# Optimization experiments

Hardware: AMD Instinct MI355X
Metric: run time of the kernel (lower is better)

## Reference

```python
import jax, jax.numpy as jnp
from jax import lax
import numpy as np

EPS = 1e-5  # BatchNorm eps


def setup_inputs() -> dict:
    key = jax.random.key(0)
    ks = jax.random.split(key, 4)
    T, B, C = 256, 128, 1024
    L, H, NCLS = 6, 1024, 1000
    x = jax.random.normal(ks[0], (T, B, C), dtype=jnp.float32)
    W = jax.random.normal(ks[1], (L, C, H), dtype=jnp.float32) * (1.0 / np.sqrt(C))
    b = jnp.zeros((L, H), dtype=jnp.float32)
    gamma = jnp.ones((L, H), dtype=jnp.float32)
    beta = jnp.zeros((L, H), dtype=jnp.float32)
    u = jax.random.uniform(ks[2], (L, H), dtype=jnp.float32)  # recurrent weights in (0, U_bound~1)
    Wc = jax.random.normal(ks[3], (H, NCLS), dtype=jnp.float32) * (1.0 / np.sqrt(H))
    bc = jnp.zeros((NCLS,), dtype=jnp.float32)
    return {"x": x, "W": W, "b": b, "gamma": gamma, "beta": beta, "u": u, "Wc": Wc, "bc": bc}


def _layer(h, Wl, bl, gl, betal, ul):
    # per-timestep dense projection: [T,B,Cin] @ [Cin,H]
    z = jnp.einsum('tbi,ih->tbh', h, Wl) + bl
    # BN over (time, batch) per channel (bn_before, training-mode batch stats)
    mean = jnp.mean(z, axis=(0, 1))
    var = jnp.var(z, axis=(0, 1))
    z = (z - mean) * (gl / jnp.sqrt(var + EPS)) + betal
    # IndRNN diagonal recurrence: h_t = relu(z_t + u * h_{t-1}), h_0 = 0
    T, B, H = z.shape
    def step(hprev, zt):
        hnew = jax.nn.relu(zt + ul * hprev)
        return hnew, hnew
    _, hs = lax.scan(step, jnp.zeros((B, H), dtype=z.dtype), z)
    return hs


def reference(x, W, b, gamma, beta, u, Wc, bc):
    h = x
    for l in range(W.shape[0]):
        h = _layer(h, W[l], b[l], gamma[l], beta[l], u[l])
    # classifier on last timestep
    return h[-1] @ Wc + bc
```

## Files before the change

### kernel.cpp

```cpp
#include <hip/hip_runtime.h>
#include <hip/hip_bf16.h>

#define T_DIM 256
#define B_DIM 128
#define C_DIM 1024
#define H_DIM 1024
#define L_DIM 6
#define NC_DIM 1000
#define M_DIM (T_DIM * B_DIM)
#define BH_DIM (B_DIM * H_DIM)

typedef __attribute__((ext_vector_type(8))) short bf16x8;
typedef __attribute__((ext_vector_type(4))) float f32x4;

__device__ __forceinline__ float bf2f(unsigned short u) {
  union { unsigned int i; float f; } v; v.i = ((unsigned int)u) << 16; return v.f;
}
__device__ __forceinline__ unsigned short f2bf(float f) {
  union { float f; unsigned int i; } v; v.f = f;
  unsigned int r = v.i + 0x7fffu + ((v.i >> 16) & 1u);
  return (unsigned short)(r >> 16);
}
__device__ __forceinline__ unsigned int pack2bf(float lo, float hi) {
  __hip_bfloat162 b2 = __float22bfloat162_rn(float2{lo, hi});
  union { __hip_bfloat162 b; unsigned int u; } cv; cv.b = b2; return cv.u;
}

__device__ __forceinline__ void gload_lds16(const void* g, void* l) {
  __builtin_amdgcn_global_load_lds(
      (const __attribute__((address_space(1))) unsigned int*)g,
      (__attribute__((address_space(3))) unsigned int*)l, 16, 0, 0);
}

__global__ __launch_bounds__(256) void f32_to_bf16_kernel(
    const float* __restrict__ in, unsigned short* __restrict__ out, int n4) {
  int stride = gridDim.x * blockDim.x;
  for (int i = blockIdx.x * blockDim.x + threadIdx.x; i < n4; i += stride) {
    float4 v = ((const float4*)in)[i];
    uint2 o; o.x = pack2bf(v.x, v.y); o.y = pack2bf(v.z, v.w);
    ((uint2*)out)[i] = o;
  }
}

__global__ __launch_bounds__(256) void wtrans_kernel(
    const float* __restrict__ W, unsigned short* __restrict__ Wt) {
  __shared__ float tile[32][33];
  int l = blockIdx.z;
  const float* Wl = W + (size_t)l * C_DIM * H_DIM;
  unsigned short* Wtl = Wt + (size_t)l * C_DIM * H_DIM;
  int h0 = blockIdx.x * 32, c0 = blockIdx.y * 32;
  int tx = threadIdx.x, ty = threadIdx.y;
#pragma unroll
  for (int i = 0; i < 32; i += 8)
    tile[ty + i][tx] = Wl[(size_t)(c0 + ty + i) * H_DIM + h0 + tx];
  __syncthreads();
#pragma unroll
  for (int i = 0; i < 32; i += 8)
    Wtl[(size_t)(h0 + ty + i) * C_DIM + c0 + tx] = f2bf(tile[tx][ty + i]);
}

#define NT 32

__global__ __launch_bounds__(512, 2) void gemm_kernel(
    const unsigned short* __restrict__ A, const unsigned short* __restrict__ Bt,
    unsigned short* __restrict__ Z, float* __restrict__ psum, float* __restrict__ psqs) {
  extern __shared__ char lds[];
  int bid = blockIdx.x;
  int swz = (bid & 7) * 32 + (bid >> 3);
  int tm0 = (swz >> 2) * 2;
  int tn = swz & 3;
  int tid = threadIdx.x;
  int wv = tid >> 6, ln = tid & 63;
  int wm = wv >> 2, wn = wv & 3;

  const char* Ap0 = (const char*)A + (size_t)tm0 * 256 * 2048;
  const char* Ap1 = Ap0 + (size_t)256 * 2048;
  const char* Bpanel = (const char*)Bt + (size_t)tn * 256 * 2048;

  int p0 = wv * 1024 + ln * 16;
  int l0 = p0 ^ (((p0 >> 7) & 3) << 4);
  size_t ro0 = (size_t)(p0 >> 6) * 2048 + (l0 & 63);
  size_t ro1 = (size_t)(128 + (p0 >> 6)) * 2048 + (l0 & 63);
  int sdst = wv * 1024;

  auto stage = [&](const char* Ap, int t) {
    char* base = lds + ((t & 3) * 32768);
    int kb = t * 64;
    gload_lds16(Ap + ro0 + kb, base + sdst);
    gload_lds16(Ap + ro1 + kb, base + 8192 + sdst);
    gload_lds16(Bpanel + ro0 + kb, base + 16384 + sdst);
    gload_lds16(Bpanel + ro1 + kb, base + 16384 + 8192 + sdst);
  };

  int frow = ln & 15;
  int fchunk = ((ln >> 4) ^ (frow >> 1)) & 3;
  int floff = frow * 64 + (fchunk << 4);

  f32x4 acc[8][4];

  bf16x8 bX[4], aP[4], aQ[4];
  auto readB_to = [&](int t, bf16x8* d) {
    const char* Bb = lds + ((t & 3) * 32768) + 16384 + wn * 4096;
#pragma unroll
    for (int n = 0; n < 4; ++n) d[n] = *(const bf16x8*)(Bb + n * 1024 + floff);
  };
  auto readA_to = [&](int t, int mq, bf16x8* d) {
    const char* Ab = lds + ((t & 3) * 32768) + wm * 8192 + mq * 4096;
#pragma unroll
    for (int i = 0; i < 4; ++i) d[i] = *(const bf16x8*)(Ab + i * 1024 + floff);
  };

  auto kloop = [&](const char* Ap) {
    f32x4 zero = {0.f, 0.f, 0.f, 0.f};
#pragma unroll
    for (int m = 0; m < 8; ++m)
#pragma unroll
      for (int n = 0; n < 4; ++n) acc[m][n] = zero;
    readB_to(0, bX); readA_to(0, 0, aP);
    for (int t = 0; t < NT; ++t) {
      readA_to(t, 1, aQ);
      if (t <= NT - 4) stage(Ap, t + 3);
      __builtin_amdgcn_s_setprio(1);
#pragma unroll
      for (int i = 0; i < 4; ++i)
#pragma unroll
        for (int n = 0; n < 4; ++n)
          acc[i][n] = __builtin_amdgcn_mfma_f32_16x16x32_bf16(aP[i], bX[n], acc[i][n], 0, 0, 0);
      __builtin_amdgcn_s_setprio(0);
      __builtin_amdgcn_s_setprio(1);
#pragma unroll
      for (int i = 0; i < 4; ++i)
#pragma unroll
        for (int n = 0; n < 4; ++n)
          acc[4 + i][n] = __builtin_amdgcn_mfma_f32_16x16x32_bf16(aQ[i], bX[n], acc[4 + i][n], 0, 0, 0);
      __builtin_amdgcn_s_setprio(0);
      if (t < NT - 1) {
        readB_to(t + 1, bX); readA_to(t + 1, 0, aP);
        if (t <= NT - 4) { asm volatile("s_waitcnt vmcnt(4)" ::: "memory"); }
        else             { asm volatile("s_waitcnt vmcnt(0)" ::: "memory"); }
        __builtin_amdgcn_s_barrier();
      }
    }
  };

  float* red = (float*)(lds + 3 * 32768);
  auto epilogue = [&](int tm) {
    float s[4], q[4];
#pragma unroll
    for (int n = 0; n < 4; ++n) {
      float sv = 0.f, qv = 0.f;
#pragma unroll
      for (int m = 0; m < 8; ++m)
#pragma unroll
        for (int r = 0; r < 4; ++r) {
          float v = acc[m][n][r];
          sv += v; qv += v * v;
        }
      s[n] = sv; q[n] = qv;
    }
#pragma unroll
    for (int n = 0; n < 4; ++n) {
      s[n] += __shfl_xor(s[n], 16); s[n] += __shfl_xor(s[n], 32);
      q[n] += __shfl_xor(q[n], 16); q[n] += __shfl_xor(q[n], 32);
    }
    if (ln < 16) {
#pragma unroll
      for (int n = 0; n < 4; ++n) {
        red[wm * 256 + wn * 64 + n * 16 + ln] = s[n];
        red[512 + wm * 256 + wn * 64 + n * 16 + ln] = q[n];
      }
    }
    __syncthreads();
    if (tid < 256) {
      psum[(size_t)tm * H_DIM + tn * 256 + tid] = red[tid] + red[256 + tid];
    } else {
      int c = tid - 256;
      psqs[(size_t)tm * H_DIM + tn * 256 + c] = red[512 + c] + red[768 + c];
    }
    __syncthreads();
    int r0 = tm * 256 + wm * 128 + ((ln >> 4) << 2);
    int c0 = tn * 256 + wn * 64 + (ln & 15);
#pragma unroll
    for (int m = 0; m < 8; ++m)
#pragma unroll
      for (int n = 0; n < 4; ++n) {
        unsigned short* zp = Z + (size_t)(r0 + m * 16) * H_DIM + c0 + n * 16;
#pragma unroll
        for (int r = 0; r < 4; ++r) zp[(size_t)r * H_DIM] = f2bf(acc[m][n][r]);
      }
  };

  stage(Ap0, 0); stage(Ap0, 1); stage(Ap0, 2);
  asm volatile("s_waitcnt vmcnt(4)" ::: "memory");
  __builtin_amdgcn_s_barrier();
  kloop(Ap0);
  __builtin_amdgcn_s_barrier();
  stage(Ap1, 0); stage(Ap1, 1); stage(Ap1, 2);
  epilogue(tm0);
  asm volatile("s_waitcnt vmcnt(4)" ::: "memory");
  __builtin_amdgcn_s_barrier();
  kloop(Ap1);
  __builtin_amdgcn_s_barrier();
  epilogue(tm0 + 1);
}

__global__ __launch_bounds__(256) void bn_finalize_kernel(
    const float* __restrict__ psum, const float* __restrict__ psqs,
    const float* __restrict__ gamma, const float* __restrict__ beta,
    float* __restrict__ ss) {
  __shared__ float sred[2][8][32];
  int c0 = blockIdx.x * 32;
  int cl = threadIdx.x & 31, jg = threadIdx.x >> 5;
  float s = 0.f, q = 0.f;
#pragma unroll
  for (int j = 0; j < 16; ++j) {
    size_t row = (size_t)(jg * 16 + j) * H_DIM + c0 + cl;
    s += psum[row];
    q += psqs[row];
  }
  sred[0][jg][cl] = s;
  sred[1][jg][cl] = q;
  __syncthreads();
  if (threadIdx.x < 32) {
    int c = threadIdx.x;
    float ts = 0.f, tq = 0.f;
#pragma unroll
    for (int g = 0; g < 8; ++g) { ts += sred[0][g][c]; tq += sred[1][g][c]; }
    const float invN = 1.0f / (float)M_DIM;
    float mean = ts * invN;
    float var = tq * invN - mean * mean;
    float sc = gamma[c0 + c] * rsqrtf(var + 1e-5f);
    ss[c0 + c] = sc;
    ss[H_DIM + c0 + c] = beta[c0 + c] - mean * sc;
  }
}

__global__ __launch_bounds__(256) void bn_recur_kernel(
    const unsigned short* __restrict__ Z, const float* __restrict__ ss,
    const float* __restrict__ u, unsigned short* __restrict__ Hout, int full) {
  int i2 = blockIdx.x * 256 + threadIdx.x;
  int h0 = (i2 & (H_DIM / 2 - 1)) * 2;
  float sc0 = ss[h0], sc1 = ss[h0 + 1];
  float sh0 = ss[H_DIM + h0], sh1 = ss[H_DIM + h0 + 1];
  float u0 = u[h0], u1 = u[h0 + 1];
  float hv0 = 0.f, hv1 = 0.f;

  const size_t ST = BH_DIM / 2;
  const unsigned int* Zt = (const unsigned int*)Z + i2;
  unsigned int* Ht = (unsigned int*)Hout + i2;

  unsigned int za[32], zb[32], ho[32];
#pragma unroll
  for (int j = 0; j < 32; ++j) za[j] = Zt[(size_t)j * ST];

#pragma unroll
  for (int blk = 0; blk < 4; ++blk) {
    int tA = blk * 64;
#pragma unroll
    for (int j = 0; j < 32; ++j) zb[j] = Zt[(size_t)(tA + 32 + j) * ST];
#pragma unroll
    for (int j = 0; j < 32; ++j) {
      unsigned int zz = za[j];
      float z0 = fmaf(bf2f((unsigned short)(zz & 0xffffu)), sc0, sh0);
      float z1 = fmaf(bf2f((unsigned short)(zz >> 16)), sc1, sh1);
      hv0 = fmaxf(fmaf(u0, hv0, z0), 0.f);
      hv1 = fmaxf(fmaf(u1, hv1, z1), 0.f);
      ho[j] = pack2bf(hv0, hv1);
    }
#pragma unroll
    for (int j = 0; j < 32; ++j)
      if (full || (tA + j) == T_DIM - 1) Ht[(size_t)(tA + j) * ST] = ho[j];
    if (blk < 3) {
#pragma unroll
      for (int j = 0; j < 32; ++j) za[j] = Zt[(size_t)(tA + 64 + j) * ST];
    }
#pragma unroll
    for (int j = 0; j < 32; ++j) {
      unsigned int zz = zb[j];
      float z0 = fmaf(bf2f((unsigned short)(zz & 0xffffu)), sc0, sh0);
      float z1 = fmaf(bf2f((unsigned short)(zz >> 16)), sc1, sh1);
      hv0 = fmaxf(fmaf(u0, hv0, z0), 0.f);
      hv1 = fmaxf(fmaf(u1, hv1, z1), 0.f);
      ho[j] = pack2bf(hv0, hv1);
    }
#pragma unroll
    for (int j = 0; j < 32; ++j)
      if (full || (tA + 32 + j) == T_DIM - 1) Ht[(size_t)(tA + 32 + j) * ST] = ho[j];
  }
}

__global__ __launch_bounds__(256) void classifier_kernel(
    const unsigned short* __restrict__ hlast, const float* __restrict__ Wc,
    const float* __restrict__ bc, float* __restrict__ out) {
  __shared__ float hs[H_DIM];
  int b = blockIdx.y;
  int n = blockIdx.x * 256 + threadIdx.x;
  for (int k = threadIdx.x; k < H_DIM; k += 256)
    hs[k] = bf2f(hlast[(size_t)b * H_DIM + k]);
  __syncthreads();
  if (n < NC_DIM) {
    float acc = bc[n];
#pragma unroll 8
    for (int k = 0; k < H_DIM; ++k)
      acc = fmaf(hs[k], Wc[(size_t)k * NC_DIM + n], acc);
    out[(size_t)b * NC_DIM + n] = acc;
  }
}

extern "C" void kernel_launch(void* const* d_in, const int* in_sizes, int n_in,
                              void* d_out, int out_size, void* d_ws, size_t ws_size,
                              hipStream_t stream) {
  const float* x     = (const float*)d_in[0];
  const float* W     = (const float*)d_in[1];
  const float* gamma = (const float*)d_in[3];
  const float* beta  = (const float*)d_in[4];
  const float* u     = (const float*)d_in[5];
  const float* Wc    = (const float*)d_in[6];
  const float* bc    = (const float*)d_in[7];
  float* out = (float*)d_out;

  const size_t CH = (size_t)C_DIM * H_DIM;
  const size_t MH = (size_t)M_DIM * H_DIM;
  char* p = (char*)d_ws;
  unsigned short* Wt = (unsigned short*)p; p += L_DIM * CH * sizeof(unsigned short);
  unsigned short* Ha = (unsigned short*)p; p += MH * sizeof(unsigned short);
  unsigned short* Hb = (unsigned short*)p; p += MH * sizeof(unsigned short);
  unsigned short* Z  = (unsigned short*)p; p += MH * sizeof(unsigned short);
  float* psum = (float*)p; p += 128 * H_DIM * sizeof(float);
  float* psqs = (float*)p; p += 128 * H_DIM * sizeof(float);
  float* ss   = (float*)p; p += 2 * H_DIM * sizeof(float);

  f32_to_bf16_kernel<<<2048, 256, 0, stream>>>(x, Ha, (int)(MH / 4));
  wtrans_kernel<<<dim3(H_DIM / 32, C_DIM / 32, L_DIM), dim3(32, 8), 0, stream>>>(W, Wt);

  unsigned short* cur = Ha;
  unsigned short* nxt = Hb;
  for (int l = 0; l < L_DIM; ++l) {
    gemm_kernel<<<256, 512, 131072, stream>>>(cur, Wt + (size_t)l * CH, Z, psum, psqs);
    bn_finalize_kernel<<<32, 256, 0, stream>>>(psum, psqs, gamma + (size_t)l * H_DIM,
                                               beta + (size_t)l * H_DIM, ss);
    bn_recur_kernel<<<BH_DIM / 512, 256, 0, stream>>>(Z, ss, u + (size_t)l * H_DIM, nxt,
                                                      (l < L_DIM - 1) ? 1 : 0);
    unsigned short* tmp = cur; cur = nxt; nxt = tmp;
  }
  classifier_kernel<<<dim3(4, B_DIM), 256, 0, stream>>>(
      cur + (size_t)(T_DIM - 1) * BH_DIM, Wc, bc, out);
}
```

Measured before the change: 694.3 us.

## Restructure GEMM into one tile per block with K=64 double-buffered quadrant pipeline

The GEMM kernel now computes one 256x256 output tile per block (512 blocks instead of 256 blocks each doing two M tiles). The K step grows to 64 with two LDS buffers of 64KB, replacing the earlier four 32KB buffers. Each K step is split into four MFMA quadrants interleaved with LDS fragment reads and half-panel global-to-LDS staging, separated by barriers and sched_barriers. A new XOR swizzle covers the 128-byte rows. The aim is better overlap of memory traffic with MFMA and fewer per-step waits, at the cost of many more barriers per iteration and less reuse of the B panel inside each block.

```diff
diff --git a/kernel.cpp b/kernel.cpp
--- a/kernel.cpp
+++ b/kernel.cpp
@@ -59,149 +59,156 @@
     Wtl[(size_t)(h0 + ty + i) * C_DIM + c0 + tx] = f2bf(tile[tx][ty + i]);
 }
 
-#define NT 32
+#define NT 16
 
 __global__ __launch_bounds__(512, 2) void gemm_kernel(
     const unsigned short* __restrict__ A, const unsigned short* __restrict__ Bt,
     unsigned short* __restrict__ Z, float* __restrict__ psum, float* __restrict__ psqs) {
   extern __shared__ char lds[];
   int bid = blockIdx.x;
-  int swz = (bid & 7) * 32 + (bid >> 3);
-  int tm0 = (swz >> 2) * 2;
-  int tn = swz & 3;
+  int swz = (bid & 7) * 64 + (bid >> 3);
+  int tm = swz >> 2, tn = swz & 3;
   int tid = threadIdx.x;
   int wv = tid >> 6, ln = tid & 63;
   int wm = wv >> 2, wn = wv & 3;
 
-  const char* Ap0 = (const char*)A + (size_t)tm0 * 256 * 2048;
-  const char* Ap1 = Ap0 + (size_t)256 * 2048;
+  const char* Apanel = (const char*)A + (size_t)tm * 256 * 2048;
   const char* Bpanel = (const char*)Bt + (size_t)tn * 256 * 2048;
 
-  int p0 = wv * 1024 + ln * 16;
-  int l0 = p0 ^ (((p0 >> 7) & 3) << 4);
-  size_t ro0 = (size_t)(p0 >> 6) * 2048 + (l0 & 63);
-  size_t ro1 = (size_t)(128 + (p0 >> 6)) * 2048 + (l0 & 63);
+  int srow = wv * 8 + (ln >> 3);
+  int sch  = (ln & 7) ^ (ln >> 3);
+  size_t goff = (size_t)srow * 2048 + sch * 16;
   int sdst = wv * 1024;
 
-  auto stage = [&](const char* Ap, int t) {
-    char* base = lds + ((t & 3) * 32768);
-    int kb = t * 64;
-    gload_lds16(Ap + ro0 + kb, base + sdst);
-    gload_lds16(Ap + ro1 + kb, base + 8192 + sdst);
-    gload_lds16(Bpanel + ro0 + kb, base + 16384 + sdst);
-    gload_lds16(Bpanel + ro1 + kb, base + 16384 + 8192 + sdst);
+  auto stageH = [&](int t, int moff, int h) {
+    char* base = lds + (t & 1) * 65536 + moff + h * 16384 + sdst;
+    const char* src = (moff ? Bpanel : Apanel) + (size_t)h * 262144 + (size_t)t * 128 + goff;
+    gload_lds16(src, base);
+    gload_lds16(src + 131072, base + 8192);
   };
 
-  int frow = ln & 15;
-  int fchunk = ((ln >> 4) ^ (frow >> 1)) & 3;
-  int floff = frow * 64 + (fchunk << 4);
+  int fr = ln & 15, fc = ln >> 4;
+  int lo0 = fr * 128 + ((fc ^ (fr & 7)) << 4);
+  int lo1 = fr * 128 + (((4 + fc) ^ (fr & 7)) << 4);
 
   f32x4 acc[8][4];
-
-  bf16x8 bX[4], aP[4], aQ[4];
-  auto readB_to = [&](int t, bf16x8* d) {
-    const char* Bb = lds + ((t & 3) * 32768) + 16384 + wn * 4096;
-#pragma unroll
-    for (int n = 0; n < 4; ++n) d[n] = *(const bf16x8*)(Bb + n * 1024 + floff);
+  f32x4 zero = {0.f, 0.f, 0.f, 0.f};
+#pragma unroll
+  for (int m = 0; m < 8; ++m)
+#pragma unroll
+    for (int n = 0; n < 4; ++n) acc[m][n] = zero;
+
+  bf16x8 Ar[4][2], B0r[2][2], B1r[2][2];
+  auto readA = [&](int t, int mh) {
+    const char* Ab = lds + (t & 1) * 65536 + wm * 16384 + mh * 8192;
+#pragma unroll
+    for (int m = 0; m < 4; ++m) {
+      Ar[m][0] = *(const bf16x8*)(Ab + m * 2048 + lo0);
+      Ar[m][1] = *(const bf16x8*)(Ab + m * 2048 + lo1);
+    }
   };
-  auto readA_to = [&](int t, int mq, bf16x8* d) {
-    const char* Ab = lds + ((t & 3) * 32768) + wm * 8192 + mq * 4096;
-#pragma unroll
-    for (int i = 0; i < 4; ++i) d[i] = *(const bf16x8*)(Ab + i * 1024 + floff);
+  auto readB = [&](int t, int nh, bf16x8 (*Br)[2]) {
+    const char* Bb = lds + (t & 1) * 65536 + 32768 + (wn >> 1) * 16384 +
+                     ((wn & 1) * 64 + nh * 32) * 128;
+#pragma unroll
+    for (int n = 0; n < 2; ++n) {
+      Br[n][0] = *(const bf16x8*)(Bb + n * 2048 + lo0);
+      Br[n][1] = *(const bf16x8*)(Bb + n * 2048 + lo1);
+    }
   };
-
-  auto kloop = [&](const char* Ap) {
-    f32x4 zero = {0.f, 0.f, 0.f, 0.f};
-#pragma unroll
-    for (int m = 0; m < 8; ++m)
-#pragma unroll
-      for (int n = 0; n < 4; ++n) acc[m][n] = zero;
-    readB_to(0, bX); readA_to(0, 0, aP);
-    for (int t = 0; t < NT; ++t) {
-      readA_to(t, 1, aQ);
-      if (t <= NT - 4) stage(Ap, t + 3);
-      __builtin_amdgcn_s_setprio(1);
-#pragma unroll
-      for (int i = 0; i < 4; ++i)
-#pragma unroll
-        for (int n = 0; n < 4; ++n)
-          acc[i][n] = __builtin_amdgcn_mfma_f32_16x16x32_bf16(aP[i], bX[n], acc[i][n], 0, 0, 0);
-      __builtin_amdgcn_s_setprio(0);
-      __builtin_amdgcn_s_setprio(1);
-#pragma unroll
-      for (int i = 0; i < 4; ++i)
-#pragma unroll
-        for (int n = 0; n < 4; ++n)
-          acc[4 + i][n] = __builtin_amdgcn_mfma_f32_16x16x32_bf16(aQ[i], bX[n], acc[4 + i][n], 0, 0, 0);
-      __builtin_amdgcn_s_setprio(0);
-      if (t < NT - 1) {
-        readB_to(t + 1, bX); readA_to(t + 1, 0, aP);
-        if (t <= NT - 4) { asm volatile("s_waitcnt vmcnt(4)" ::: "memory"); }
-        else             { asm volatile("s_waitcnt vmcnt(0)" ::: "memory"); }
-        __builtin_amdgcn_s_barrier();
-      }
-    }
+  auto mfmaQ = [&](int mh, int nh, bf16x8 (*Br)[2]) {
+    __builtin_amdgcn_s_setprio(1);
+#pragma unroll
+    for (int m = 0; m < 4; ++m)
+#pragma unroll
+      for (int n = 0; n < 2; ++n)
+#pragma unroll
+        for (int kk = 0; kk < 2; ++kk)
+          acc[mh * 4 + m][nh * 2 + n] = __builtin_amdgcn_mfma_f32_16x16x32_bf16(
+              Ar[m][kk], Br[n][kk], acc[mh * 4 + m][nh * 2 + n], 0, 0, 0);
+    __builtin_amdgcn_s_setprio(0);
   };
 
-  float* red = (float*)(lds + 3 * 32768);
-  auto epilogue = [&](int tm) {
-    float s[4], q[4];
-#pragma unroll
-    for (int n = 0; n < 4; ++n) {
-      float sv = 0.f, qv = 0.f;
-#pragma unroll
-      for (int m = 0; m < 8; ++m)
-#pragma unroll
-        for (int r = 0; r < 4; ++r) {
-          float v = acc[m][n][r];
-          sv += v; qv += v * v;
-        }
-      s[n] = sv; q[n] = qv;
-    }
-#pragma unroll
-    for (int n = 0; n < 4; ++n) {
-      s[n] += __shfl_xor(s[n], 16); s[n] += __shfl_xor(s[n], 32);
-      q[n] += __shfl_xor(q[n], 16); q[n] += __shfl_xor(q[n], 32);
-    }
-    if (ln < 16) {
-#pragma unroll
-      for (int n = 0; n < 4; ++n) {
-        red[wm * 256 + wn * 64 + n * 16 + ln] = s[n];
-        red[512 + wm * 256 + wn * 64 + n * 16 + ln] = q[n];
-      }
-    }
-    __syncthreads();
-    if (tid < 256) {
-      psum[(size_t)tm * H_DIM + tn * 256 + tid] = red[tid] + red[256 + tid];
-    } else {
-      int c = tid - 256;
-      psqs[(size_t)tm * H_DIM + tn * 256 + c] = red[512 + c] + red[768 + c];
-    }
-    __syncthreads();
-    int r0 = tm * 256 + wm * 128 + ((ln >> 4) << 2);
-    int c0 = tn * 256 + wn * 64 + (ln & 15);
-#pragma unroll
-    for (int m = 0; m < 8; ++m)
-#pragma unroll
-      for (int n = 0; n < 4; ++n) {
-        unsigned short* zp = Z + (size_t)(r0 + m * 16) * H_DIM + c0 + n * 16;
-#pragma unroll
-        for (int r = 0; r < 4; ++r) zp[(size_t)r * H_DIM] = f2bf(acc[m][n][r]);
-      }
-  };
-
-  stage(Ap0, 0); stage(Ap0, 1); stage(Ap0, 2);
+  stageH(0, 0, 0); stageH(0, 0, 1); stageH(0, 32768, 0); stageH(0, 32768, 1);
+  stageH(1, 32768, 0); stageH(1, 32768, 1);
   asm volatile("s_waitcnt vmcnt(4)" ::: "memory");
   __builtin_amdgcn_s_barrier();
-  kloop(Ap0);
-  __builtin_amdgcn_s_barrier();
-  stage(Ap1, 0); stage(Ap1, 1); stage(Ap1, 2);
-  epilogue(tm0);
-  asm volatile("s_waitcnt vmcnt(4)" ::: "memory");
-  __builtin_amdgcn_s_barrier();
-  kloop(Ap1);
-  __builtin_amdgcn_s_barrier();
-  epilogue(tm0 + 1);
+
+  for (int tt = 0; tt < NT; ++tt) {
+    readA(tt, 0); readB(tt, 0, B0r);
+    if (tt + 1 < NT) stageH(tt + 1, 0, 0);
+    asm volatile("s_waitcnt lgkmcnt(8)" ::: "memory");
+    __builtin_amdgcn_s_barrier();
+    asm volatile("s_waitcnt lgkmcnt(0)" ::: "memory");
+    __builtin_amdgcn_sched_barrier(0);
+    mfmaQ(0, 0, B0r);
+    __builtin_amdgcn_s_barrier();
+    readB(tt, 1, B1r);
+    if (tt + 1 < NT) stageH(tt + 1, 0, 1);
+    __builtin_amdgcn_s_barrier();
+    asm volatile("s_waitcnt lgkmcnt(0)" ::: "memory");
+    __builtin_amdgcn_sched_barrier(0);
+    mfmaQ(0, 1, B1r);
+    __builtin_amdgcn_s_barrier();
+    readA(tt, 1);
+    if (tt + 2 < NT) stageH(tt + 2, 32768, 0);
+    __builtin_amdgcn_s_barrier();
+    asm volatile("s_waitcnt lgkmcnt(0)" ::: "memory");
+    __builtin_amdgcn_sched_barrier(0);
+    mfmaQ(1, 1, B1r);
+    __builtin_amdgcn_s_barrier();
+    if (tt + 2 < NT) stageH(tt + 2, 32768, 1);
+    __builtin_amdgcn_s_barrier();
+    __builtin_amdgcn_sched_barrier(0);
+    mfmaQ(1, 0, B0r);
+    if (tt + 2 < NT) { asm volatile("s_waitcnt vmcnt(4)" ::: "memory"); }
+    else             { asm volatile("s_waitcnt vmcnt(0)" ::: "memory"); }
+    __builtin_amdgcn_s_barrier();
+  }
+
+  float s[4], q[4];
+#pragma unroll
+  for (int n = 0; n < 4; ++n) {
+    float sv = 0.f, qv = 0.f;
+#pragma unroll
+    for (int m = 0; m < 8; ++m)
+#pragma unroll
+      for (int r = 0; r < 4; ++r) {
+        float v = acc[m][n][r];
+        sv += v; qv += v * v;
+      }
+    s[n] = sv; q[n] = qv;
+  }
+#pragma unroll
+  for (int n = 0; n < 4; ++n) {
+    s[n] += __shfl_xor(s[n], 16); s[n] += __shfl_xor(s[n], 32);
+    q[n] += __shfl_xor(q[n], 16); q[n] += __shfl_xor(q[n], 32);
+  }
+  float* red = (float*)lds;
+  if (ln < 16) {
+#pragma unroll
+    for (int n = 0; n < 4; ++n) {
+      red[wm * 256 + wn * 64 + n * 16 + ln] = s[n];
+      red[512 + wm * 256 + wn * 64 + n * 16 + ln] = q[n];
+    }
+  }
+  __syncthreads();
+  if (tid < 256) {
+    psum[(size_t)tm * H_DIM + tn * 256 + tid] = red[tid] + red[256 + tid];
+  } else {
+    int c = tid - 256;
+    psqs[(size_t)tm * H_DIM + tn * 256 + c] = red[512 + c] + red[768 + c];
+  }
+  int r0 = tm * 256 + wm * 128 + ((ln >> 4) << 2);
+  int c0 = tn * 256 + wn * 64 + (ln & 15);
+#pragma unroll
+  for (int m = 0; m < 8; ++m)
+#pragma unroll
+    for (int n = 0; n < 4; ++n) {
+      unsigned short* zp = Z + (size_t)(r0 + m * 16) * H_DIM + c0 + n * 16;
+#pragma unroll
+      for (int r = 0; r < 4; ++r) zp[(size_t)r * H_DIM] = f2bf(acc[m][n][r]);
+    }
 }
 
 __global__ __launch_bounds__(256) void bn_finalize_kernel(
@@ -336,7 +343,8 @@
   unsigned short* cur = Ha;
   unsigned short* nxt = Hb;
   for (int l = 0; l < L_DIM; ++l) {
-    gemm_kernel<<<256, 512, 131072, stream>>>(cur, Wt + (size_t)l * CH, Z, psum, psqs);
+    gemm_kernel<<<(M_DIM / 256) * (H_DIM / 256), 512, 131072, stream>>>(
+        cur, Wt + (size_t)l * CH, Z, psum, psqs);
     bn_finalize_kernel<<<32, 256, 0, stream>>>(psum, psqs, gamma + (size_t)l * H_DIM,
                                                beta + (size_t)l * H_DIM, ss);
     bn_recur_kernel<<<BH_DIM / 512, 256, 0, stream>>>(Z, ss, u + (size_t)l * H_DIM, nxt,
```

Result: faster. 661.4 us (-4.7%).
